# Kernel optimization log

Measured on AMD Instinct MI355X. Metric: run time of the kernel, lower is better.

Reference implementation:

```python
import jax, jax.numpy as jnp
import numpy as np

WINDOW = 33  # must match init_kwargs window_size (odd)


def setup_inputs() -> dict:
    key = jax.random.key(0)
    kq, kk, kv, km = jax.random.split(key, 4)
    B, S, D = 4, 2048, 256
    query = jax.random.normal(kq, (B, S, D), dtype=jnp.float32)
    k = jax.random.normal(kk, (B, S, D), dtype=jnp.float32)
    value = jax.random.normal(kv, (B, S, D), dtype=jnp.float32)
    mask = jax.random.randint(km, (B, S), 0, 2).astype(jnp.int32)
    return {"query": query, "key": k, "value": value, "mask": mask}


def reference(query, key, value, mask):
    # Local (sliding-window) attention, window centered at each position.
    B, S, D = query.shape
    half = WINDOW // 2
    offs = jnp.arange(-half, half + 1)                 # [W]
    idx = jnp.arange(S)[:, None] + offs[None, :]       # [S, W]
    valid = (idx >= 0) & (idx < S)                     # in-bounds window entries
    idxc = jnp.clip(idx, 0, S - 1)
    k_win = key[:, idxc]                               # [B, S, W, D]
    v_win = value[:, idxc]                             # [B, S, W, D]
    scores = jnp.einsum('bsd,bswd->bsw', query, k_win) / jnp.sqrt(jnp.float32(D))
    m_win = (mask[:, idxc] != 0) & valid[None]         # [B, S, W]
    scores = jnp.where(m_win, scores, jnp.float32(-1e10))  # masked_fill(-1e10)
    p_attn = jax.nn.softmax(scores, axis=-1)           # [B, S, W]
    values = jnp.einsum('bsw,bswd->bsd', p_attn, v_win)
    return values, p_attn
```

## Files before the change

kernel.cpp:

```cpp
#include <hip/hip_runtime.h>
#include <math.h>

#define S_LEN 2048
#define D_DIM 256
#define WIN 33
#define HALF 16
#define PT_STRIDE 72

typedef __attribute__((ext_vector_type(8))) short short8_t;
typedef __attribute__((ext_vector_type(4))) float f32x4;

__device__ inline unsigned short f32_to_bf16(float f) {
    unsigned u = __float_as_uint(f);
    return (unsigned short)((u + 0x7fffu + ((u >> 16) & 1u)) >> 16);
}

__device__ inline short8_t pack_bf16x8(float4 a, float4 b) {
    short8_t r;
    r[0] = (short)f32_to_bf16(a.x); r[1] = (short)f32_to_bf16(a.y);
    r[2] = (short)f32_to_bf16(a.z); r[3] = (short)f32_to_bf16(a.w);
    r[4] = (short)f32_to_bf16(b.x); r[5] = (short)f32_to_bf16(b.y);
    r[6] = (short)f32_to_bf16(b.z); r[7] = (short)f32_to_bf16(b.w);
    return r;
}

__global__ __launch_bounds__(128) void local_attn_wv(
    const float* __restrict__ q,
    const float* __restrict__ k,
    const float* __restrict__ v,
    const int*   __restrict__ mask,
    float* __restrict__ out_v,
    float* __restrict__ out_p)
{
    __shared__ __align__(16) unsigned short Pt[16 * PT_STRIDE];

    const int t    = threadIdx.x;
    const int lane = t & 63;
    const int h    = t >> 6;
    const int l15  = lane & 15;
    const int q4   = lane >> 4;

    const int tile = blockIdx.x;
    const int b    = tile >> 7;
    const int s0   = (tile & 127) << 4;

    const float* qb = q + ((size_t)b * S_LEN + s0) * D_DIM;
    const float* kb = k + (size_t)b * S_LEN * D_DIM;
    const float* vb = v + (size_t)b * S_LEN * D_DIM;

    if (h == 0) {
        int  krow[3]; bool mv[3];
#pragma unroll
        for (int ct = 0; ct < 3; ++ct) {
            const int kv    = s0 - HALF + ct * 16 + l15;
            const bool valid = (kv >= 0) && (kv < S_LEN);
            const int kc    = min(max(kv, 0), S_LEN - 1);
            krow[ct] = kc;
            mv[ct]   = valid && (mask[b * S_LEN + kc] != 0);
        }
        short8_t aq[8];
#pragma unroll
        for (int ks = 0; ks < 8; ++ks) {
            const float* p = qb + l15 * D_DIM + ks * 32 + q4 * 8;
            const float4 x = *(const float4*)p;
            const float4 y = *(const float4*)(p + 4);
            aq[ks] = pack_bf16x8(x, y);
        }
        f32x4 acc[3];
        acc[0] = (f32x4){0.f,0.f,0.f,0.f};
        acc[1] = (f32x4){0.f,0.f,0.f,0.f};
        acc[2] = (f32x4){0.f,0.f,0.f,0.f};
#pragma unroll
        for (int ct = 0; ct < 3; ++ct) {
            const float* kr = kb + (size_t)krow[ct] * D_DIM;
#pragma unroll
            for (int ks = 0; ks < 8; ++ks) {
                const float* p = kr + ks * 32 + q4 * 8;
                const float4 x = *(const float4*)p;
                const float4 y = *(const float4*)(p + 4);
                const short8_t bk = pack_bf16x8(x, y);
                acc[ct] = __builtin_amdgcn_mfma_f32_16x16x32_bf16(aq[ks], bk, acc[ct], 0, 0, 0);
            }
        }
        float sv[3][4];
#pragma unroll
        for (int ct = 0; ct < 3; ++ct)
#pragma unroll
            for (int r = 0; r < 4; ++r) {
                const int m = q4 * 4 + r;
                const int c = ct * 16 + l15;
                const int j = c - m;
                const bool inband = (j >= 0) && (j < WIN);
                const float s = acc[ct][r] * 0.0625f;
                sv[ct][r] = inband ? (mv[ct] ? s : -1e10f) : -1e30f;
            }
        float rmax[4], rinv[4];
#pragma unroll
        for (int r = 0; r < 4; ++r) {
            float m = fmaxf(fmaxf(sv[0][r], sv[1][r]), sv[2][r]);
            m = fmaxf(m, __shfl_xor(m, 1, 64));
            m = fmaxf(m, __shfl_xor(m, 2, 64));
            m = fmaxf(m, __shfl_xor(m, 4, 64));
            m = fmaxf(m, __shfl_xor(m, 8, 64));
            rmax[r] = m;
        }
#pragma unroll
        for (int ct = 0; ct < 3; ++ct)
#pragma unroll
            for (int r = 0; r < 4; ++r)
                sv[ct][r] = __expf(sv[ct][r] - rmax[r]);
#pragma unroll
        for (int r = 0; r < 4; ++r) {
            float s = sv[0][r] + sv[1][r] + sv[2][r];
            s += __shfl_xor(s, 1, 64);
            s += __shfl_xor(s, 2, 64);
            s += __shfl_xor(s, 4, 64);
            s += __shfl_xor(s, 8, 64);
            rinv[r] = 1.0f / s;
        }
#pragma unroll
        for (int ct = 0; ct < 3; ++ct)
#pragma unroll
            for (int r = 0; r < 4; ++r) {
                const int m = q4 * 4 + r;
                const int c = ct * 16 + l15;
                const float p = sv[ct][r] * rinv[r];
                Pt[m * PT_STRIDE + c] = f32_to_bf16(p);
                const int j = c - m;
                if (j >= 0 && j < WIN)
                    out_p[((size_t)(b * S_LEN + s0 + m)) * WIN + j] = p;
            }
#pragma unroll
        for (int r = 0; r < 4; ++r)
            Pt[(q4 * 4 + r) * PT_STRIDE + 48 + l15] = 0;
    }
    __syncthreads();

    short8_t ap[2];
#pragma unroll
    for (int ks = 0; ks < 2; ++ks)
        ap[ks] = *(const short8_t*)&Pt[l15 * PT_STRIDE + ks * 32 + q4 * 8];

    const float* vrow[2][8];
#pragma unroll
    for (int ks = 0; ks < 2; ++ks)
#pragma unroll
        for (int j = 0; j < 8; ++j) {
            const int g  = ks * 32 + q4 * 8 + j;
            const int kv = min(max(s0 - HALF + g, 0), S_LEN - 1);
            vrow[ks][j] = vb + (size_t)kv * D_DIM + h * 128;
        }

    f32x4 acc[8];
#pragma unroll
    for (int nt = 0; nt < 8; ++nt) acc[nt] = (f32x4){0.f,0.f,0.f,0.f};
#pragma unroll
    for (int nt = 0; nt < 8; ++nt) {
        const int d = nt * 16 + l15;
#pragma unroll
        for (int ks = 0; ks < 2; ++ks) {
            float4 x, y;
            x.x = vrow[ks][0][d]; x.y = vrow[ks][1][d];
            x.z = vrow[ks][2][d]; x.w = vrow[ks][3][d];
            y.x = vrow[ks][4][d]; y.y = vrow[ks][5][d];
            y.z = vrow[ks][6][d]; y.w = vrow[ks][7][d];
            const short8_t bv = pack_bf16x8(x, y);
            acc[nt] = __builtin_amdgcn_mfma_f32_16x16x32_bf16(ap[ks], bv, acc[nt], 0, 0, 0);
        }
    }
    float* ob = out_v + ((size_t)b * S_LEN + s0) * D_DIM + h * 128;
#pragma unroll
    for (int nt = 0; nt < 8; ++nt)
#pragma unroll
        for (int r = 0; r < 4; ++r)
            ob[(size_t)(q4 * 4 + r) * D_DIM + nt * 16 + l15] = acc[nt][r];
}

extern "C" void kernel_launch(void* const* d_in, const int* in_sizes, int n_in,
                              void* d_out, int out_size, void* d_ws, size_t ws_size,
                              hipStream_t stream) {
    const float* q    = (const float*)d_in[0];
    const float* k    = (const float*)d_in[1];
    const float* v    = (const float*)d_in[2];
    const int*   mask = (const int*)d_in[3];

    const int B = 4;
    float* out_v = (float*)d_out;
    float* out_p = (float*)d_out + (size_t)B * S_LEN * D_DIM;

    const int blocks = B * (S_LEN / 16);
    local_attn_wv<<<blocks, 128, 0, stream>>>(q, k, v, mask, out_v, out_p);
}
```

Measured before the change: 84.32 us.

## Prefetch V fragments before barrier, skip padded rows, remap tiles, cheaper bf16 pack

V window rows are loaded and packed into bf16 registers before the __syncthreads, so both waves fetch V while wave 0 is still computing the softmax. Lanes whose second K-slice covers only padded window rows (q4>=2) skip those loads and use a zero fragment. Block indices are permuted so consecutive blocks spread across batches and sequence positions. The bf16 conversion becomes two adds plus one byte-perm per pair, which rounds half-up instead of round-to-nearest-even and slightly changes precision. Holding 16 packed fragments per thread raises register pressure.

After: 84.73 us. About the same (+0.5%).

```diff
diff --git a/kernel.cpp b/kernel.cpp
--- a/kernel.cpp
+++ b/kernel.cpp
@@ -15,13 +15,19 @@
     return (unsigned short)((u + 0x7fffu + ((u >> 16) & 1u)) >> 16);
 }
 
-__device__ inline short8_t pack_bf16x8(float4 a, float4 b) {
-    short8_t r;
-    r[0] = (short)f32_to_bf16(a.x); r[1] = (short)f32_to_bf16(a.y);
-    r[2] = (short)f32_to_bf16(a.z); r[3] = (short)f32_to_bf16(a.w);
-    r[4] = (short)f32_to_bf16(b.x); r[5] = (short)f32_to_bf16(b.y);
-    r[6] = (short)f32_to_bf16(b.z); r[7] = (short)f32_to_bf16(b.w);
-    return r;
+__device__ inline unsigned pack2_bf16(float lo, float hi) {
+    unsigned a = __float_as_uint(lo) + 0x8000u;
+    unsigned b = __float_as_uint(hi) + 0x8000u;
+    return __builtin_amdgcn_perm(b, a, 0x07060302);
+}
+
+__device__ inline short8_t pack_bf16x8(float4 x, float4 y) {
+    union { unsigned u[4]; short8_t s; } r;
+    r.u[0] = pack2_bf16(x.x, x.y);
+    r.u[1] = pack2_bf16(x.z, x.w);
+    r.u[2] = pack2_bf16(y.x, y.y);
+    r.u[3] = pack2_bf16(y.z, y.w);
+    return r.s;
 }
 
 __global__ __launch_bounds__(128) void local_attn_wv(
@@ -40,7 +46,8 @@
     const int l15  = lane & 15;
     const int q4   = lane >> 4;
 
-    const int tile = blockIdx.x;
+    const int bid  = blockIdx.x;
+    const int tile = ((bid & 7) << 6) | (bid >> 3);
     const int b    = tile >> 7;
     const int s0   = (tile & 127) << 4;
 
@@ -134,39 +141,51 @@
         for (int r = 0; r < 4; ++r)
             Pt[(q4 * 4 + r) * PT_STRIDE + 48 + l15] = 0;
     }
+
+    short8_t bv[8][2];
+    {
+        const float* vrk0[8];
+        const float* vrk1[8];
+#pragma unroll
+        for (int j = 0; j < 8; ++j) {
+            const int g0 = q4 * 8 + j;
+            const int g1 = 32 + q4 * 8 + j;
+            const int kv0 = min(max(s0 - HALF + g0, 0), S_LEN - 1);
+            const int kv1 = min(max(s0 - HALF + g1, 0), S_LEN - 1);
+            vrk0[j] = vb + (size_t)kv0 * D_DIM + h * 128;
+            vrk1[j] = vb + (size_t)kv1 * D_DIM + h * 128;
+        }
+        const bool act1 = (q4 < 2);
+        const short8_t zfrag = {0,0,0,0,0,0,0,0};
+#pragma unroll
+        for (int nt = 0; nt < 8; ++nt) {
+            const int d = nt * 16 + l15;
+            float4 x, y;
+            x.x = vrk0[0][d]; x.y = vrk0[1][d]; x.z = vrk0[2][d]; x.w = vrk0[3][d];
+            y.x = vrk0[4][d]; y.y = vrk0[5][d]; y.z = vrk0[6][d]; y.w = vrk0[7][d];
+            bv[nt][0] = pack_bf16x8(x, y);
+            if (act1) {
+                x.x = vrk1[0][d]; x.y = vrk1[1][d]; x.z = vrk1[2][d]; x.w = vrk1[3][d];
+                y.x = vrk1[4][d]; y.y = vrk1[5][d]; y.z = vrk1[6][d]; y.w = vrk1[7][d];
+                bv[nt][1] = pack_bf16x8(x, y);
+            } else {
+                bv[nt][1] = zfrag;
+            }
+        }
+    }
     __syncthreads();
 
     short8_t ap[2];
-#pragma unroll
-    for (int ks = 0; ks < 2; ++ks)
-        ap[ks] = *(const short8_t*)&Pt[l15 * PT_STRIDE + ks * 32 + q4 * 8];
-
-    const float* vrow[2][8];
-#pragma unroll
-    for (int ks = 0; ks < 2; ++ks)
-#pragma unroll
-        for (int j = 0; j < 8; ++j) {
-            const int g  = ks * 32 + q4 * 8 + j;
-            const int kv = min(max(s0 - HALF + g, 0), S_LEN - 1);
-            vrow[ks][j] = vb + (size_t)kv * D_DIM + h * 128;
-        }
+    ap[0] = *(const short8_t*)&Pt[l15 * PT_STRIDE + q4 * 8];
+    ap[1] = *(const short8_t*)&Pt[l15 * PT_STRIDE + 32 + q4 * 8];
 
     f32x4 acc[8];
 #pragma unroll
     for (int nt = 0; nt < 8; ++nt) acc[nt] = (f32x4){0.f,0.f,0.f,0.f};
 #pragma unroll
     for (int nt = 0; nt < 8; ++nt) {
-        const int d = nt * 16 + l15;
-#pragma unroll
-        for (int ks = 0; ks < 2; ++ks) {
-            float4 x, y;
-            x.x = vrow[ks][0][d]; x.y = vrow[ks][1][d];
-            x.z = vrow[ks][2][d]; x.w = vrow[ks][3][d];
-            y.x = vrow[ks][4][d]; y.y = vrow[ks][5][d];
-            y.z = vrow[ks][6][d]; y.w = vrow[ks][7][d];
-            const short8_t bv = pack_bf16x8(x, y);
-            acc[nt] = __builtin_amdgcn_mfma_f32_16x16x32_bf16(ap[ks], bv, acc[nt], 0, 0, 0);
-        }
+        acc[nt] = __builtin_amdgcn_mfma_f32_16x16x32_bf16(ap[0], bv[nt][0], acc[nt], 0, 0, 0);
+        acc[nt] = __builtin_amdgcn_mfma_f32_16x16x32_bf16(ap[1], bv[nt][1], acc[nt], 0, 0, 0);
     }
     float* ob = out_v + ((size_t)b * S_LEN + s0) * D_DIM + h * 128;
 #pragma unroll
```
